# Optimization experiments

Hardware: AMD Instinct MI355X
Metric: run time of the kernel (lower is better)

The kernel has to match this reference:

```python
import jax, jax.numpy as jnp
import numpy as np

B, H, W, C = 8, 64, 64, 256
CK = C // 8  # key/query dim of conv_f / conv_g


def setup_inputs() -> dict:
    key = jax.random.key(0)
    ks = jax.random.split(key, 10)
    s = lambda fan_in: 1.0 / np.sqrt(fan_in)
    return {
        "x": jax.random.normal(ks[0], (B, H, W, C), dtype=jnp.float32),
        "Wf": jax.random.normal(ks[1], (C, CK), dtype=jnp.float32) * s(C),
        "bf": jnp.zeros((CK,), dtype=jnp.float32),
        "Wg": jax.random.normal(ks[2], (C, CK), dtype=jnp.float32) * s(C),
        "bg": jnp.zeros((CK,), dtype=jnp.float32),
        "Wh": jax.random.normal(ks[3], (C, C), dtype=jnp.float32) * s(C),
        "bh": jnp.zeros((C,), dtype=jnp.float32),
        "Wo": jax.random.normal(ks[4], (C, C), dtype=jnp.float32) * s(C),
        "bo": jnp.zeros((C,), dtype=jnp.float32),
        # original init is zeros; use a random scalar so output/grads are nontrivial
        "gamma": jax.random.normal(ks[5], (1,), dtype=jnp.float32),
    }


def reference(x, Wf, bf, Wg, bg, Wh, bh, Wo, bo, gamma):
    b, h, w, c = x.shape
    n = h * w
    xf = x.reshape(b, n, c)                       # flatten spatial: [B, N, C]
    # 1x1 convs == per-pixel matmuls
    f = xf @ Wf + bf                              # [B, N, C//8]
    g = xf @ Wg + bg                              # [B, N, C//8]
    hh = xf @ Wh + bh                             # [B, N, C]
    # scores[b, i, j] = <g_i, f_j>; softmax over j (keys)
    scores = jnp.einsum("bnd,bmd->bnm", g, f)     # [B, N, N]
    attn = jax.nn.softmax(scores, axis=-1)
    o = jnp.einsum("bnm,bmc->bnc", attn, hh)      # [B, N, C]
    o = o @ Wo + bo                               # conv_o (1x1)
    out = gamma * o + xf                          # gamma residual
    return out.reshape(b, h, w, c)
```

## Files before the change

### kernel.cpp

```cpp
#include <hip/hip_runtime.h>
#include <hip/hip_fp16.h>
#include <hip/hip_bf16.h>

constexpr int BB  = 8;
constexpr int NN  = 4096;
constexpr int CC  = 256;
constexpr int CKK = 32;

typedef __attribute__((ext_vector_type(8))) short    short8;
typedef __attribute__((ext_vector_type(8))) _Float16 half8;
typedef __attribute__((ext_vector_type(4))) _Float16 half4;
typedef __attribute__((ext_vector_type(4))) float    f32x4;

__device__ __forceinline__ unsigned short bf16_bits(float v) {
    __hip_bfloat16 h = __float2bfloat16(v);
    return *reinterpret_cast<unsigned short*>(&h);
}
__device__ __forceinline__ float bf16_val(unsigned short u) {
    __hip_bfloat16 h = *reinterpret_cast<__hip_bfloat16*>(&u);
    return __bfloat162float(h);
}

__global__ __launch_bounds__(256) void prep_kernel(
    const float* __restrict__ Wf, const float* __restrict__ Wg,
    const float* __restrict__ Wh, const float* __restrict__ Wo,
    unsigned short* __restrict__ WThi, unsigned short* __restrict__ WTlo)
{
    const int n = blockIdx.x;
    const int k = threadIdx.x;
    float v;
    if      (n < 256) v = Wh[k * 256 + n];
    else if (n < 288) v = Wf[k * 32 + (n - 256)];
    else if (n < 320) v = Wg[k * 32 + (n - 288)];
    else              v = Wo[k * 256 + (n - 320)];
    const unsigned short hi = bf16_bits(v);
    WThi[n * 256 + k] = hi;
    WTlo[n * 256 + k] = bf16_bits(v - bf16_val(hi));
}

__global__ __launch_bounds__(256) void fgh_kernel(
    const float* __restrict__ x,
    const unsigned short* __restrict__ WThi, const unsigned short* __restrict__ WTlo,
    const float* __restrict__ bf, const float* __restrict__ bg,
    const float* __restrict__ bh,
    _Float16* __restrict__ fbuf, _Float16* __restrict__ gbuf,
    _Float16* __restrict__ hhT)
{
    const int tid = threadIdx.x, w = tid >> 6, lane = tid & 63;
    const int ln = lane & 15, lq = lane >> 4;
    const int px0 = blockIdx.x * 256 + w * 64;
    const int n0  = blockIdx.y * 64;

    f32x4 acc[4][4];
    #pragma unroll
    for (int i = 0; i < 4; ++i)
        #pragma unroll
        for (int j = 0; j < 4; ++j) acc[i][j] = {0.f, 0.f, 0.f, 0.f};

    #pragma unroll 1
    for (int kc = 0; kc < 8; ++kc) {
        const int k0 = kc * 32;
        short8 Ahi[4], Alo[4];
        #pragma unroll
        for (int mt = 0; mt < 4; ++mt) {
            float av[8];
            const float* xp = &x[(size_t)(px0 + mt * 16 + ln) * CC + k0 + lq * 8];
            *(float4*)&av[0] = *(const float4*)xp;
            *(float4*)&av[4] = *(const float4*)(xp + 4);
            #pragma unroll
            for (int j = 0; j < 8; ++j) {
                const unsigned short h = bf16_bits(av[j]);
                Ahi[mt][j] = (short)h;
                Alo[mt][j] = (short)bf16_bits(av[j] - bf16_val(h));
            }
        }
        #pragma unroll
        for (int nt = 0; nt < 4; ++nt) {
            const size_t boff = (size_t)(n0 + nt * 16 + ln) * 256 + k0 + lq * 8;
            const short8 Bhi = *(const short8*)&WThi[boff];
            const short8 Blo = *(const short8*)&WTlo[boff];
            #pragma unroll
            for (int mt = 0; mt < 4; ++mt) {
                acc[mt][nt] = __builtin_amdgcn_mfma_f32_16x16x32_bf16(Ahi[mt], Bhi, acc[mt][nt], 0, 0, 0);
                acc[mt][nt] = __builtin_amdgcn_mfma_f32_16x16x32_bf16(Ahi[mt], Blo, acc[mt][nt], 0, 0, 0);
                acc[mt][nt] = __builtin_amdgcn_mfma_f32_16x16x32_bf16(Alo[mt], Bhi, acc[mt][nt], 0, 0, 0);
            }
        }
    }

    const int b = px0 >> 12;
    if (blockIdx.y < 4) {
        #pragma unroll
        for (int nt = 0; nt < 4; ++nt) {
            const int c = n0 + nt * 16 + ln;
            const float bias = bh[c];
            #pragma unroll
            for (int mt = 0; mt < 4; ++mt) {
                half4 hv;
                #pragma unroll
                for (int r = 0; r < 4; ++r) hv[r] = (_Float16)(acc[mt][nt][r] + bias);
                const int npix = (px0 & (NN - 1)) + mt * 16 + lq * 4;
                *(half4*)&hhT[((size_t)(b * CC + c)) * NN + npix] = hv;
            }
        }
    } else {
        #pragma unroll
        for (int nt = 0; nt < 4; ++nt) {
            const int d = (nt & 1) * 16 + ln;
            const float bias = (nt < 2) ? bf[d] : bg[d];
            _Float16* dst = (nt < 2) ? fbuf : gbuf;
            #pragma unroll
            for (int mt = 0; mt < 4; ++mt)
                #pragma unroll
                for (int r = 0; r < 4; ++r)
                    dst[(size_t)(px0 + mt * 16 + lq * 4 + r) * CKK + d] =
                        (_Float16)(acc[mt][nt][r] + bias);
        }
    }
}

__global__ __launch_bounds__(256, 2) void attn_kernel(
    const _Float16* __restrict__ fbuf, const _Float16* __restrict__ gbuf,
    const _Float16* __restrict__ hhT, float* __restrict__ obuf)
{
    __shared__ _Float16 P[2][64 * 72];
    __shared__ float mxbuf[4][64];
    __shared__ float rsbuf[4][64];

    const int tid = threadIdx.x, w = tid >> 6, lane = tid & 63;
    const int ln = lane & 15, lq = lane >> 4;
    const int b  = blockIdx.x & 7;
    const int q0 = (blockIdx.x >> 3) * 64;
    const int cb = w * 64;

    const f32x4 zero = {0.f, 0.f, 0.f, 0.f};
    constexpr float LOG2E = 1.4426950408889634f;

    half8 Bg[4];
    #pragma unroll
    for (int qt = 0; qt < 4; ++qt)
        Bg[qt] = *(const half8*)&gbuf[(size_t)(b * NN + q0 + qt * 16 + ln) * CKK + lq * 8];

    const _Float16* fb = &fbuf[(size_t)(b * NN + w * 16 + ln) * CKK + lq * 8];
    const _Float16* hb = &hhT[((size_t)(b * CC + cb + ln)) * NN + lq * 8];

    float mx[4];
    #pragma unroll
    for (int qt = 0; qt < 4; ++qt) mx[qt] = -1e30f;
    half8 Afc = *(const half8*)fb;
    #pragma unroll 1
    for (int j0 = 0; j0 < NN; j0 += 64) {
        const int jn = (j0 + 64 < NN) ? j0 + 64 : j0;
        const half8 Afn = *(const half8*)&fb[(size_t)jn * CKK];
        #pragma unroll
        for (int qt = 0; qt < 4; ++qt) {
            const f32x4 s = __builtin_amdgcn_mfma_f32_16x16x32_f16(Afc, Bg[qt], zero, 0, 0, 0);
            mx[qt] = fmaxf(mx[qt], fmaxf(fmaxf(s[0], s[1]), fmaxf(s[2], s[3])));
        }
        Afc = Afn;
    }
    #pragma unroll
    for (int qt = 0; qt < 4; ++qt) {
        mx[qt] = fmaxf(mx[qt], __shfl_xor(mx[qt], 16));
        mx[qt] = fmaxf(mx[qt], __shfl_xor(mx[qt], 32));
    }
    if (lane < 16) {
        #pragma unroll
        for (int qt = 0; qt < 4; ++qt) mxbuf[w][qt * 16 + ln] = mx[qt];
    }
    __syncthreads();
    float mk[4];
    #pragma unroll
    for (int qt = 0; qt < 4; ++qt)
        mk[qt] = LOG2E * fmaxf(fmaxf(mxbuf[0][qt * 16 + ln], mxbuf[1][qt * 16 + ln]),
                               fmaxf(mxbuf[2][qt * 16 + ln], mxbuf[3][qt * 16 + ln]));

    f32x4 O[4][4];
    #pragma unroll
    for (int qt = 0; qt < 4; ++qt)
        #pragma unroll
        for (int ct = 0; ct < 4; ++ct) O[qt][ct] = zero;
    float psum[4] = {0.f, 0.f, 0.f, 0.f};

    auto phaseA = [&](const half8& Af, _Float16* Pb) {
        #pragma unroll
        for (int qt = 0; qt < 4; ++qt) {
            const f32x4 s = __builtin_amdgcn_mfma_f32_16x16x32_f16(Af, Bg[qt], zero, 0, 0, 0);
            half4 ph;
            float ps = 0.f;
            #pragma unroll
            for (int r = 0; r < 4; ++r) {
                const float p = exp2f(fmaf(s[r], LOG2E, -mk[qt]));
                ps += p;
                ph[r] = (_Float16)p;
            }
            psum[qt] += ps;
            *(half4*)&Pb[(qt * 16 + ln) * 72 + w * 16 + lq * 4] = ph;
        }
    };

    auto loadBh = [&](half8 (&Bh)[4][2], int j0) {
        #pragma unroll
        for (int ct = 0; ct < 4; ++ct)
            #pragma unroll
            for (int kh = 0; kh < 2; ++kh)
                Bh[ct][kh] = *(const half8*)&hb[(size_t)ct * 16 * NN + j0 + kh * 32];
    };

    auto phaseB = [&](const half8 (&Bh)[4][2], const _Float16* Pb) {
        __builtin_amdgcn_s_setprio(1);
        #pragma unroll
        for (int qt = 0; qt < 4; ++qt) {
            const half8 Ap0 = *(const half8*)&Pb[(qt * 16 + ln) * 72 + lq * 8];
            const half8 Ap1 = *(const half8*)&Pb[(qt * 16 + ln) * 72 + 32 + lq * 8];
            #pragma unroll
            for (int ct = 0; ct < 4; ++ct) {
                O[qt][ct] = __builtin_amdgcn_mfma_f32_16x16x32_f16(Ap0, Bh[ct][0], O[qt][ct], 0, 0, 0);
                O[qt][ct] = __builtin_amdgcn_mfma_f32_16x16x32_f16(Ap1, Bh[ct][1], O[qt][ct], 0, 0, 0);
            }
        }
        __builtin_amdgcn_s_setprio(0);
    };

    half8 Bh0[4][2], Bh1[4][2];
    half8 Af0, Af1;
    loadBh(Bh0, 0);
    Af0 = *(const half8*)fb;

    #pragma unroll 1
    for (int j0 = 0; j0 < NN; j0 += 128) {
        phaseA(Af0, P[0]);
        __syncthreads();
        loadBh(Bh1, j0 + 64);
        Af1 = *(const half8*)&fb[(size_t)(j0 + 64) * CKK];
        phaseB(Bh0, P[0]);
        phaseA(Af1, P[1]);
        __syncthreads();
        if (j0 + 128 < NN) {
            loadBh(Bh0, j0 + 128);
            Af0 = *(const half8*)&fb[(size_t)(j0 + 128) * CKK];
        }
        phaseB(Bh1, P[1]);
    }

    #pragma unroll
    for (int qt = 0; qt < 4; ++qt) {
        psum[qt] += __shfl_xor(psum[qt], 16);
        psum[qt] += __shfl_xor(psum[qt], 32);
    }
    if (lane < 16) {
        #pragma unroll
        for (int qt = 0; qt < 4; ++qt) rsbuf[w][qt * 16 + ln] = psum[qt];
    }
    __syncthreads();

    #pragma unroll
    for (int qt = 0; qt < 4; ++qt)
        #pragma unroll
        for (int r = 0; r < 4; ++r) {
            const int q = qt * 16 + lq * 4 + r;
            const float rinv = 1.0f / (rsbuf[0][q] + rsbuf[1][q] + rsbuf[2][q] + rsbuf[3][q]);
            #pragma unroll
            for (int ct = 0; ct < 4; ++ct)
                obuf[((size_t)(b * NN + q0 + q)) * CC + cb + ct * 16 + ln] = O[qt][ct][r] * rinv;
        }
}

__global__ __launch_bounds__(256) void out_kernel(
    const float* __restrict__ obuf,
    const unsigned short* __restrict__ WThi, const unsigned short* __restrict__ WTlo,
    const float* __restrict__ bo, const float* __restrict__ gamma,
    const float* __restrict__ x, float* __restrict__ out)
{
    const int tid = threadIdx.x, w = tid >> 6, lane = tid & 63;
    const int ln = lane & 15, lq = lane >> 4;
    const int px0 = blockIdx.x * 256 + w * 64;
    const int n0  = blockIdx.y * 64;

    f32x4 acc[4][4];
    #pragma unroll
    for (int i = 0; i < 4; ++i)
        #pragma unroll
        for (int j = 0; j < 4; ++j) acc[i][j] = {0.f, 0.f, 0.f, 0.f};

    #pragma unroll 1
    for (int kc = 0; kc < 8; ++kc) {
        const int k0 = kc * 32;
        short8 Ahi[4], Alo[4];
        #pragma unroll
        for (int mt = 0; mt < 4; ++mt) {
            float av[8];
            const float* op = &obuf[(size_t)(px0 + mt * 16 + ln) * CC + k0 + lq * 8];
            *(float4*)&av[0] = *(const float4*)op;
            *(float4*)&av[4] = *(const float4*)(op + 4);
            #pragma unroll
            for (int j = 0; j < 8; ++j) {
                const unsigned short h = bf16_bits(av[j]);
                Ahi[mt][j] = (short)h;
                Alo[mt][j] = (short)bf16_bits(av[j] - bf16_val(h));
            }
        }
        #pragma unroll
        for (int nt = 0; nt < 4; ++nt) {
            const size_t boff = (size_t)(320 + n0 + nt * 16 + ln) * 256 + k0 + lq * 8;
            const short8 Bhi = *(const short8*)&WThi[boff];
            const short8 Blo = *(const short8*)&WTlo[boff];
            #pragma unroll
            for (int mt = 0; mt < 4; ++mt) {
                acc[mt][nt] = __builtin_amdgcn_mfma_f32_16x16x32_bf16(Ahi[mt], Bhi, acc[mt][nt], 0, 0, 0);
                acc[mt][nt] = __builtin_amdgcn_mfma_f32_16x16x32_bf16(Ahi[mt], Blo, acc[mt][nt], 0, 0, 0);
                acc[mt][nt] = __builtin_amdgcn_mfma_f32_16x16x32_bf16(Alo[mt], Bhi, acc[mt][nt], 0, 0, 0);
            }
        }
    }

    const float gm = gamma[0];
    #pragma unroll
    for (int nt = 0; nt < 4; ++nt) {
        const int c = n0 + nt * 16 + ln;
        const float bias = bo[c];
        #pragma unroll
        for (int mt = 0; mt < 4; ++mt)
            #pragma unroll
            for (int r = 0; r < 4; ++r) {
                const size_t idx = (size_t)(px0 + mt * 16 + lq * 4 + r) * CC + c;
                out[idx] = gm * (acc[mt][nt][r] + bias) + x[idx];
            }
    }
}

extern "C" void kernel_launch(void* const* d_in, const int* in_sizes, int n_in,
                              void* d_out, int out_size, void* d_ws, size_t ws_size,
                              hipStream_t stream)
{
    (void)in_sizes; (void)n_in; (void)out_size; (void)ws_size;

    const float* x     = (const float*)d_in[0];
    const float* Wf    = (const float*)d_in[1];
    const float* bf    = (const float*)d_in[2];
    const float* Wg    = (const float*)d_in[3];
    const float* bg    = (const float*)d_in[4];
    const float* Wh    = (const float*)d_in[5];
    const float* bh    = (const float*)d_in[6];
    const float* Wo    = (const float*)d_in[7];
    const float* bo    = (const float*)d_in[8];
    const float* gamma = (const float*)d_in[9];
    float* out = (float*)d_out;

    _Float16* fbuf = (_Float16*)d_ws;
    _Float16* gbuf = fbuf + (size_t)BB * NN * CKK;
    _Float16* hhT  = gbuf + (size_t)BB * NN * CKK;
    float*    obuf = (float*)(hhT + (size_t)BB * CC * NN);
    unsigned short* WThi = (unsigned short*)(obuf + (size_t)BB * NN * CC);
    unsigned short* WTlo = WThi + (size_t)576 * 256;

    prep_kernel<<<576, 256, 0, stream>>>(Wf, Wg, Wh, Wo, WThi, WTlo);
    fgh_kernel<<<dim3(BB * NN / 256, 5), 256, 0, stream>>>(x, WThi, WTlo, bf, bg, bh,
                                                           fbuf, gbuf, hhT);
    attn_kernel<<<BB * NN / 64, 256, 0, stream>>>(fbuf, gbuf, hhT, obuf);
    out_kernel<<<dim3(BB * NN / 256, 4), 256, 0, stream>>>(obuf, WThi, WTlo, bo, gamma, x, out);
}
```

Measured before the change: 328.9 us.

## Fuse output projection into attention kernel and merge fgh column blocks

The conv_o projection and gamma residual now run at the end of the attention kernel. The normalized attention output is staged in shared memory (reusing the P buffers' space) instead of a global fp32 buffer, which removes a full write/read of the intermediate and one kernel launch. The fgh projection kernel now computes all 320 output columns per 64-pixel block, so x is read once instead of once per column group. The cost is larger shared memory use per attention block, which may limit occupancy, and a longer serial epilogue.

```diff
diff --git a/kernel.cpp b/kernel.cpp
--- a/kernel.cpp
+++ b/kernel.cpp
@@ -48,23 +48,25 @@
 {
     const int tid = threadIdx.x, w = tid >> 6, lane = tid & 63;
     const int ln = lane & 15, lq = lane >> 4;
-    const int px0 = blockIdx.x * 256 + w * 64;
-    const int n0  = blockIdx.y * 64;
-
-    f32x4 acc[4][4];
+    const int b  = blockIdx.x & 7;
+    const int q0 = (blockIdx.x >> 3) * 64;
+    const size_t px0 = (size_t)b * NN + q0;
+    const int n0 = w * 80;
+
+    f32x4 acc[4][5];
     #pragma unroll
     for (int i = 0; i < 4; ++i)
         #pragma unroll
-        for (int j = 0; j < 4; ++j) acc[i][j] = {0.f, 0.f, 0.f, 0.f};
-
+        for (int j = 0; j < 5; ++j) acc[i][j] = {0.f, 0.f, 0.f, 0.f};
+
+    short8 Ahi[4], Alo[4];
     #pragma unroll 1
     for (int kc = 0; kc < 8; ++kc) {
         const int k0 = kc * 32;
-        short8 Ahi[4], Alo[4];
         #pragma unroll
         for (int mt = 0; mt < 4; ++mt) {
             float av[8];
-            const float* xp = &x[(size_t)(px0 + mt * 16 + ln) * CC + k0 + lq * 8];
+            const float* xp = &x[(px0 + mt * 16 + ln) * CC + k0 + lq * 8];
             *(float4*)&av[0] = *(const float4*)xp;
             *(float4*)&av[4] = *(const float4*)(xp + 4);
             #pragma unroll
@@ -75,7 +77,7 @@
             }
         }
         #pragma unroll
-        for (int nt = 0; nt < 4; ++nt) {
+        for (int nt = 0; nt < 5; ++nt) {
             const size_t boff = (size_t)(n0 + nt * 16 + ln) * 256 + k0 + lq * 8;
             const short8 Bhi = *(const short8*)&WThi[boff];
             const short8 Blo = *(const short8*)&WTlo[boff];
@@ -88,32 +90,28 @@
         }
     }
 
-    const int b = px0 >> 12;
-    if (blockIdx.y < 4) {
-        #pragma unroll
-        for (int nt = 0; nt < 4; ++nt) {
-            const int c = n0 + nt * 16 + ln;
+    #pragma unroll
+    for (int nt = 0; nt < 5; ++nt) {
+        const int c = n0 + nt * 16 + ln;
+        if (c < 256) {
             const float bias = bh[c];
             #pragma unroll
             for (int mt = 0; mt < 4; ++mt) {
                 half4 hv;
                 #pragma unroll
                 for (int r = 0; r < 4; ++r) hv[r] = (_Float16)(acc[mt][nt][r] + bias);
-                const int npix = (px0 & (NN - 1)) + mt * 16 + lq * 4;
-                *(half4*)&hhT[((size_t)(b * CC + c)) * NN + npix] = hv;
-            }
-        }
-    } else {
-        #pragma unroll
-        for (int nt = 0; nt < 4; ++nt) {
-            const int d = (nt & 1) * 16 + ln;
-            const float bias = (nt < 2) ? bf[d] : bg[d];
-            _Float16* dst = (nt < 2) ? fbuf : gbuf;
+                *(half4*)&hhT[((size_t)(b * CC + c)) * NN + q0 + mt * 16 + lq * 4] = hv;
+            }
+        } else {
+            const bool isf = (c < 288);
+            const int d = isf ? (c - 256) : (c - 288);
+            const float bias = isf ? bf[d] : bg[d];
+            _Float16* dst = isf ? fbuf : gbuf;
             #pragma unroll
             for (int mt = 0; mt < 4; ++mt)
                 #pragma unroll
                 for (int r = 0; r < 4; ++r)
-                    dst[(size_t)(px0 + mt * 16 + lq * 4 + r) * CKK + d] =
+                    dst[(px0 + mt * 16 + lq * 4 + r) * CKK + d] =
                         (_Float16)(acc[mt][nt][r] + bias);
         }
     }
@@ -121,9 +119,14 @@
 
 __global__ __launch_bounds__(256, 2) void attn_kernel(
     const _Float16* __restrict__ fbuf, const _Float16* __restrict__ gbuf,
-    const _Float16* __restrict__ hhT, float* __restrict__ obuf)
+    const _Float16* __restrict__ hhT,
+    const unsigned short* __restrict__ WThi, const unsigned short* __restrict__ WTlo,
+    const float* __restrict__ bo, const float* __restrict__ gamma,
+    const float* __restrict__ x, float* __restrict__ out)
 {
-    __shared__ _Float16 P[2][64 * 72];
+    __shared__ __align__(16) float OF[64 * 268];
+    _Float16* P0 = (_Float16*)OF;
+    _Float16* P1 = P0 + 64 * 72;
     __shared__ float mxbuf[4][64];
     __shared__ float rsbuf[4][64];
 
@@ -229,18 +232,18 @@
 
     #pragma unroll 1
     for (int j0 = 0; j0 < NN; j0 += 128) {
-        phaseA(Af0, P[0]);
+        phaseA(Af0, P0);
         __syncthreads();
         loadBh(Bh1, j0 + 64);
         Af1 = *(const half8*)&fb[(size_t)(j0 + 64) * CKK];
-        phaseB(Bh0, P[0]);
-        phaseA(Af1, P[1]);
+        phaseB(Bh0, P0);
+        phaseA(Af1, P1);
         __syncthreads();
         if (j0 + 128 < NN) {
             loadBh(Bh0, j0 + 128);
             Af0 = *(const half8*)&fb[(size_t)(j0 + 128) * CKK];
         }
-        phaseB(Bh1, P[1]);
+        phaseB(Bh1, P1);
     }
 
     #pragma unroll
@@ -262,70 +265,61 @@
             const float rinv = 1.0f / (rsbuf[0][q] + rsbuf[1][q] + rsbuf[2][q] + rsbuf[3][q]);
             #pragma unroll
             for (int ct = 0; ct < 4; ++ct)
-                obuf[((size_t)(b * NN + q0 + q)) * CC + cb + ct * 16 + ln] = O[qt][ct][r] * rinv;
-        }
-}
-
-__global__ __launch_bounds__(256) void out_kernel(
-    const float* __restrict__ obuf,
-    const unsigned short* __restrict__ WThi, const unsigned short* __restrict__ WTlo,
-    const float* __restrict__ bo, const float* __restrict__ gamma,
-    const float* __restrict__ x, float* __restrict__ out)
-{
-    const int tid = threadIdx.x, w = tid >> 6, lane = tid & 63;
-    const int ln = lane & 15, lq = lane >> 4;
-    const int px0 = blockIdx.x * 256 + w * 64;
-    const int n0  = blockIdx.y * 64;
-
-    f32x4 acc[4][4];
-    #pragma unroll
-    for (int i = 0; i < 4; ++i)
-        #pragma unroll
-        for (int j = 0; j < 4; ++j) acc[i][j] = {0.f, 0.f, 0.f, 0.f};
-
-    #pragma unroll 1
-    for (int kc = 0; kc < 8; ++kc) {
-        const int k0 = kc * 32;
+                OF[q * 268 + cb + ct * 16 + ln] = O[qt][ct][r] * rinv;
+        }
+    __syncthreads();
+
+    {
+        const int n0 = w * 64;
+        f32x4 acc[4][4];
+        #pragma unroll
+        for (int i = 0; i < 4; ++i)
+            #pragma unroll
+            for (int j = 0; j < 4; ++j) acc[i][j] = {0.f, 0.f, 0.f, 0.f};
+
         short8 Ahi[4], Alo[4];
-        #pragma unroll
-        for (int mt = 0; mt < 4; ++mt) {
-            float av[8];
-            const float* op = &obuf[(size_t)(px0 + mt * 16 + ln) * CC + k0 + lq * 8];
-            *(float4*)&av[0] = *(const float4*)op;
-            *(float4*)&av[4] = *(const float4*)(op + 4);
-            #pragma unroll
-            for (int j = 0; j < 8; ++j) {
-                const unsigned short h = bf16_bits(av[j]);
-                Ahi[mt][j] = (short)h;
-                Alo[mt][j] = (short)bf16_bits(av[j] - bf16_val(h));
-            }
-        }
+        #pragma unroll 1
+        for (int kc = 0; kc < 8; ++kc) {
+            const int k0 = kc * 32;
+            #pragma unroll
+            for (int mt = 0; mt < 4; ++mt) {
+                float av[8];
+                *(f32x4*)&av[0] = *(const f32x4*)&OF[(mt * 16 + ln) * 268 + k0 + lq * 8];
+                *(f32x4*)&av[4] = *(const f32x4*)&OF[(mt * 16 + ln) * 268 + k0 + lq * 8 + 4];
+                #pragma unroll
+                for (int j = 0; j < 8; ++j) {
+                    const unsigned short h = bf16_bits(av[j]);
+                    Ahi[mt][j] = (short)h;
+                    Alo[mt][j] = (short)bf16_bits(av[j] - bf16_val(h));
+                }
+            }
+            #pragma unroll
+            for (int nt = 0; nt < 4; ++nt) {
+                const size_t boff = (size_t)(320 + n0 + nt * 16 + ln) * 256 + k0 + lq * 8;
+                const short8 Bhi = *(const short8*)&WThi[boff];
+                const short8 Blo = *(const short8*)&WTlo[boff];
+                #pragma unroll
+                for (int mt = 0; mt < 4; ++mt) {
+                    acc[mt][nt] = __builtin_amdgcn_mfma_f32_16x16x32_bf16(Ahi[mt], Bhi, acc[mt][nt], 0, 0, 0);
+                    acc[mt][nt] = __builtin_amdgcn_mfma_f32_16x16x32_bf16(Ahi[mt], Blo, acc[mt][nt], 0, 0, 0);
+                    acc[mt][nt] = __builtin_amdgcn_mfma_f32_16x16x32_bf16(Alo[mt], Bhi, acc[mt][nt], 0, 0, 0);
+                }
+            }
+        }
+
+        const float gm = gamma[0];
         #pragma unroll
         for (int nt = 0; nt < 4; ++nt) {
-            const size_t boff = (size_t)(320 + n0 + nt * 16 + ln) * 256 + k0 + lq * 8;
-            const short8 Bhi = *(const short8*)&WThi[boff];
-            const short8 Blo = *(const short8*)&WTlo[boff];
-            #pragma unroll
-            for (int mt = 0; mt < 4; ++mt) {
-                acc[mt][nt] = __builtin_amdgcn_mfma_f32_16x16x32_bf16(Ahi[mt], Bhi, acc[mt][nt], 0, 0, 0);
-                acc[mt][nt] = __builtin_amdgcn_mfma_f32_16x16x32_bf16(Ahi[mt], Blo, acc[mt][nt], 0, 0, 0);
-                acc[mt][nt] = __builtin_amdgcn_mfma_f32_16x16x32_bf16(Alo[mt], Bhi, acc[mt][nt], 0, 0, 0);
-            }
-        }
-    }
-
-    const float gm = gamma[0];
-    #pragma unroll
-    for (int nt = 0; nt < 4; ++nt) {
-        const int c = n0 + nt * 16 + ln;
-        const float bias = bo[c];
-        #pragma unroll
-        for (int mt = 0; mt < 4; ++mt)
-            #pragma unroll
-            for (int r = 0; r < 4; ++r) {
-                const size_t idx = (size_t)(px0 + mt * 16 + lq * 4 + r) * CC + c;
-                out[idx] = gm * (acc[mt][nt][r] + bias) + x[idx];
-            }
+            const int c = n0 + nt * 16 + ln;
+            const float bias = bo[c];
+            #pragma unroll
+            for (int mt = 0; mt < 4; ++mt)
+                #pragma unroll
+                for (int r = 0; r < 4; ++r) {
+                    const size_t idx = (size_t)(b * NN + q0 + mt * 16 + lq * 4 + r) * CC + c;
+                    out[idx] = gm * (acc[mt][nt][r] + bias) + x[idx];
+                }
+        }
     }
 }
 
@@ -350,13 +344,12 @@
     _Float16* fbuf = (_Float16*)d_ws;
     _Float16* gbuf = fbuf + (size_t)BB * NN * CKK;
     _Float16* hhT  = gbuf + (size_t)BB * NN * CKK;
-    float*    obuf = (float*)(hhT + (size_t)BB * CC * NN);
-    unsigned short* WThi = (unsigned short*)(obuf + (size_t)BB * NN * CC);
+    unsigned short* WThi = (unsigned short*)(hhT + (size_t)BB * CC * NN);
     unsigned short* WTlo = WThi + (size_t)576 * 256;
 
     prep_kernel<<<576, 256, 0, stream>>>(Wf, Wg, Wh, Wo, WThi, WTlo);
-    fgh_kernel<<<dim3(BB * NN / 256, 5), 256, 0, stream>>>(x, WThi, WTlo, bf, bg, bh,
-                                                           fbuf, gbuf, hhT);
-    attn_kernel<<<BB * NN / 64, 256, 0, stream>>>(fbuf, gbuf, hhT, obuf);
-    out_kernel<<<dim3(BB * NN / 256, 4), 256, 0, stream>>>(obuf, WThi, WTlo, bo, gamma, x, out);
-}
+    fgh_kernel<<<BB * NN / 64, 256, 0, stream>>>(x, WThi, WTlo, bf, bg, bh,
+                                                 fbuf, gbuf, hhT);
+    attn_kernel<<<BB * NN / 64, 256, 0, stream>>>(fbuf, gbuf, hhT, WThi, WTlo,
+                                                  bo, gamma, x, out);
+}
```

Measured after the change: 298.8 us. 1.1x faster.
